# Kernel tuning notes

Hardware: AMD Instinct MI355X
Metric: run time of the kernel (lower is better)

The kernel has to match this reference:

```python
import jax, jax.numpy as jnp
import numpy as np

N_CONCEPTS = 32
D_MODEL = 512
COMMITMENT_COST = 0.25


def setup_inputs() -> dict:
    key = jax.random.key(0)
    kx, kc = jax.random.split(key)
    x = jax.random.normal(kx, (8, 8192, D_MODEL), dtype=jnp.float32)
    codebook = jax.random.normal(kc, (N_CONCEPTS, D_MODEL), dtype=jnp.float32) * 0.02
    return {"x": x, "codebook": codebook}


def reference(x, codebook):
    B, T, D = x.shape
    x_flat = x.reshape(B * T, D)
    x2 = jnp.sum(x_flat * x_flat, axis=1, keepdims=True)          # [BT,1]
    c2 = jnp.sum(codebook * codebook, axis=1)                      # [K]
    xc = jnp.einsum('nd,kd->nk', x_flat, codebook)                 # [BT,K]
    dists = x2 + c2 - 2.0 * xc
    nearest_idx = jnp.argmin(dists, axis=1)                        # [BT]
    q = codebook[nearest_idx]                                      # gather [BT,D]
    # straight-through estimator
    quantized = x_flat + jax.lax.stop_gradient(q - x_flat)
    vq_loss = (jnp.mean((jax.lax.stop_gradient(quantized) - x_flat) ** 2)
               + COMMITMENT_COST * jnp.mean((quantized - jax.lax.stop_gradient(x_flat)) ** 2))
    # histogram of concept usage (fused replacement of the per-concept loop)
    counts = jnp.zeros((N_CONCEPTS,), dtype=jnp.int32).at[nearest_idx].add(1)
    return quantized.reshape(B, T, D), vq_loss, counts
```

## Files before the change

### kernel.cpp

```cpp
#include <hip/hip_runtime.h>

#define BT_ROWS 65536
#define DIM     512
#define NK      32
#define TPB     64
#define RPB     32
#define NBLK    (BT_ROWS / RPB)
#define CHUNK   32
#define NCHUNK  (DIM / CHUNK)
#define DQ      3

typedef float f4 __attribute__((ext_vector_type(4)));
typedef float f32x16 __attribute__((ext_vector_type(16)));
typedef short bf16x8 __attribute__((ext_vector_type(8)));
typedef unsigned int u32x4 __attribute__((ext_vector_type(4)));

union Frag { u32x4 q; unsigned int w[4]; bf16x8 v; };


__global__ void vq_prep(const float* __restrict__ cb, float* __restrict__ c2,
                        int* __restrict__ counts, unsigned int* __restrict__ cbh32) {
    int t = threadIdx.x;
    const f4* c4 = (const f4*)cb;
#pragma unroll
    for (int i = 0; i < 16; ++i) {
        f4 v = c4[t * 16 + i];
        unsigned int w0, w1;
        asm("v_cvt_pk_bf16_f32 %0, %1, %2" : "=v"(w0) : "v"(v.x), "v"(v.y));
        asm("v_cvt_pk_bf16_f32 %0, %1, %2" : "=v"(w1) : "v"(v.z), "v"(v.w));
        cbh32[t * 32 + 2 * i]     = w0;
        cbh32[t * 32 + 2 * i + 1] = w1;
    }
    if (t < NK) {
        float s = 0.f;
#pragma unroll 8
        for (int i = 0; i < DIM / 4; ++i) {
            f4 v = c4[t * (DIM / 4) + i];
            s += v.x * v.x + v.y * v.y + v.z * v.z + v.w * v.w;
        }
        c2[t] = s;
    } else if (t < 2 * NK) {
        counts[t - NK] = 0;
    }
}

__global__ __launch_bounds__(TPB, 2) void vq_main(const float* __restrict__ x,
                                                  const float* __restrict__ cb,
                                                  const float* __restrict__ c2,
                                                  const unsigned short* __restrict__ cbh,
                                                  float* __restrict__ out,
                                                  float* __restrict__ blockloss,
                                                  int* __restrict__ counts) {
    const int lane = threadIdx.x & 63;
    const int n    = lane & 31;
    const int hi   = lane >> 5;
    const int R0   = blockIdx.x * RPB;

    const char* xb = (const char*)x + (size_t)(R0 + n) * (DIM * 4) + hi * 32;
    const unsigned short* cbn = cbh + (size_t)n * DIM + hi * 8;

    f4   rs[DQ][4];
    Frag fr[DQ][2];
#define GLOAD(c) do {                                                    \
    rs[(c) % DQ][0] = *(const f4*)(xb + (c) * 128);                      \
    rs[(c) % DQ][1] = *(const f4*)(xb + (c) * 128 + 16);                 \
    rs[(c) % DQ][2] = *(const f4*)(xb + (c) * 128 + 64);                 \
    rs[(c) % DQ][3] = *(const f4*)(xb + (c) * 128 + 80);                 \
    fr[(c) % DQ][0].q = *(const u32x4*)(cbn + (c) * CHUNK);              \
    fr[(c) % DQ][1].q = *(const u32x4*)(cbn + (c) * CHUNK + 16);         \
} while (0)

    f32x16 acc;
#pragma unroll
    for (int r = 0; r < 16; ++r) acc[r] = 0.f;
    float x2acc = 0.f;

    GLOAD(0); GLOAD(1); GLOAD(2);

#pragma unroll
    for (int c = 0; c < NCHUNK; ++c) {
        f4   a0 = rs[c % DQ][0], a1 = rs[c % DQ][1];
        f4   a2 = rs[c % DQ][2], a3 = rs[c % DQ][3];
        Frag f0 = fr[c % DQ][0], f1 = fr[c % DQ][1];
        if (c + DQ < NCHUNK) GLOAD(c + DQ);

        x2acc += a0.x * a0.x + a0.y * a0.y + a0.z * a0.z + a0.w * a0.w
               + a1.x * a1.x + a1.y * a1.y + a1.z * a1.z + a1.w * a1.w
               + a2.x * a2.x + a2.y * a2.y + a2.z * a2.z + a2.w * a2.w
               + a3.x * a3.x + a3.y * a3.y + a3.z * a3.z + a3.w * a3.w;

        Frag fa;
        asm("v_cvt_pk_bf16_f32 %0, %1, %2" : "=v"(fa.w[0]) : "v"(a0.x), "v"(a0.y));
        asm("v_cvt_pk_bf16_f32 %0, %1, %2" : "=v"(fa.w[1]) : "v"(a0.z), "v"(a0.w));
        asm("v_cvt_pk_bf16_f32 %0, %1, %2" : "=v"(fa.w[2]) : "v"(a1.x), "v"(a1.y));
        asm("v_cvt_pk_bf16_f32 %0, %1, %2" : "=v"(fa.w[3]) : "v"(a1.z), "v"(a1.w));
        acc = __builtin_amdgcn_mfma_f32_32x32x16_bf16(fa.v, f0.v, acc, 0, 0, 0);

        Frag fb;
        asm("v_cvt_pk_bf16_f32 %0, %1, %2" : "=v"(fb.w[0]) : "v"(a2.x), "v"(a2.y));
        asm("v_cvt_pk_bf16_f32 %0, %1, %2" : "=v"(fb.w[1]) : "v"(a2.z), "v"(a2.w));
        asm("v_cvt_pk_bf16_f32 %0, %1, %2" : "=v"(fb.w[2]) : "v"(a3.x), "v"(a3.y));
        asm("v_cvt_pk_bf16_f32 %0, %1, %2" : "=v"(fb.w[3]) : "v"(a3.z), "v"(a3.w));
        acc = __builtin_amdgcn_mfma_f32_32x32x16_bf16(fb.v, f1.v, acc, 0, 0, 0);
    }
#undef GLOAD

    float x2tot = x2acc;
#pragma unroll
    for (int mo = 1; mo <= 32; mo <<= 1) x2tot += __shfl_xor(x2tot, mo, 64);

    const float c2v = c2[n];
    float val[16]; int idx[16];
#pragma unroll
    for (int r = 0; r < 16; ++r) {
        val[r] = c2v - 2.f * acc[r];
        idx[r] = n;
#pragma unroll
        for (int off = 1; off <= 16; off <<= 1) {
            float ov = __shfl_xor(val[r], off, 64);
            int   oi = __shfl_xor(idx[r], off, 64);
            if (ov < val[r] || (ov == val[r] && oi < idx[r])) { val[r] = ov; idx[r] = oi; }
        }
    }

    float lsum = 0.f;
#pragma unroll
    for (int r = 0; r < 16; ++r) lsum += val[r];
    float lother = __shfl(lsum, 32, 64);
    if (lane == 0) blockloss[blockIdx.x] = x2tot + lsum + lother;

    const f4* __restrict__ cb4 = (const f4*)cb;
    f4* __restrict__ o4 = (f4*)out;
    int cnt = 0;
#pragma unroll
    for (int rr = 0; rr < 32; ++rr) {
        const int r = (rr & 3) | (((rr >> 3) & 3) << 2);
        const int h = (rr >> 2) & 1;
        int kr = __shfl(idx[r], h << 5, 64);
        cnt += (kr == n) ? 1 : 0;
        size_t base = (size_t)(R0 + rr) * (DIM / 4);
        o4[base + lane]      = cb4[kr * (DIM / 4) + lane];
        o4[base + 64 + lane] = cb4[kr * (DIM / 4) + 64 + lane];
    }
    if (hi == 0 && cnt) atomicAdd(&counts[n], cnt);

__asm__ volatile("" ::: "memory");
}

__global__ void vq_final(const float* __restrict__ blockloss, const int* __restrict__ counts,
                         float* __restrict__ out) {
    int   t = threadIdx.x;
    float v = 0.f;
#pragma unroll
    for (int i = 0; i < NBLK / 256; ++i) v += blockloss[t + i * 256];
#pragma unroll
    for (int m = 32; m; m >>= 1) v += __shfl_xor(v, m, 64);
    __shared__ float red[4];
    if ((t & 63) == 0) red[t >> 6] = v;
    __syncthreads();
    if (t == 0)
        out[(size_t)BT_ROWS * DIM] =
            1.25f * (red[0] + red[1] + red[2] + red[3]) / (float)((size_t)BT_ROWS * DIM);
    if (t < NK)
        out[(size_t)BT_ROWS * DIM + 1 + t] = (float)counts[t];
}

extern "C" void kernel_launch(void* const* d_in, const int* in_sizes, int n_in,
                              void* d_out, int out_size, void* d_ws, size_t ws_size,
                              hipStream_t stream) {
    const float* x  = (const float*)d_in[0];
    const float* cb = (const float*)d_in[1];
    float* out = (float*)d_out;

    float* f         = (float*)d_ws;
    float* c2        = f;
    float* blockloss = f + NK;
    int*   counts    = (int*)(f + NK + NBLK);
    unsigned int*   cbh32 = (unsigned int*)((char*)d_ws + 16384);
    unsigned short* cbh   = (unsigned short*)cbh32;

    vq_prep<<<1, 256, 0, stream>>>(cb, c2, counts, cbh32);
    vq_main<<<NBLK, TPB, 0, stream>>>(x, cb, c2, cbh, out, blockloss, counts);
    vq_final<<<1, 256, 0, stream>>>(blockloss, counts, out);
}
```

Before: 72.31 us.

## Split reduction dimension across four waves per block and combine via LDS

Each block now runs four wavefronts, each computing MFMA partial dot products over a quarter of the feature dimension. Three waves write their partial accumulators and squared-norm sums to shared memory, and wave 0 combines them before doing the argmin and loss. The gather/write of quantized rows is then split across all four waves using indices passed through shared memory. This raises parallelism and memory-level concurrency per row tile, at the cost of LDS traffic, two block barriers, and a serial section in which only one wave works.

After: 141.2 us. 95.2% more time.

```diff
diff --git a/kernel.cpp b/kernel.cpp
--- a/kernel.cpp
+++ b/kernel.cpp
@@ -3,11 +3,11 @@
 #define BT_ROWS 65536
 #define DIM     512
 #define NK      32
-#define TPB     64
+#define TPB     256
 #define RPB     32
 #define NBLK    (BT_ROWS / RPB)
 #define CHUNK   32
-#define NCHUNK  (DIM / CHUNK)
+#define NCW     4
 #define DQ      3
 
 typedef float f4 __attribute__((ext_vector_type(4)));
@@ -44,20 +44,25 @@
     }
 }
 
-__global__ __launch_bounds__(TPB, 2) void vq_main(const float* __restrict__ x,
+__global__ __launch_bounds__(TPB, 8) void vq_main(const float* __restrict__ x,
                                                   const float* __restrict__ cb,
                                                   const float* __restrict__ c2,
                                                   const unsigned short* __restrict__ cbh,
                                                   float* __restrict__ out,
                                                   float* __restrict__ blockloss,
                                                   int* __restrict__ counts) {
-    const int lane = threadIdx.x & 63;
+    const int tid  = threadIdx.x;
+    const int lane = tid & 63;
+    const int wv   = tid >> 6;
     const int n    = lane & 31;
     const int hi   = lane >> 5;
     const int R0   = blockIdx.x * RPB;
 
-    const char* xb = (const char*)x + (size_t)(R0 + n) * (DIM * 4) + hi * 32;
-    const unsigned short* cbn = cbh + (size_t)n * DIM + hi * 8;
+    __shared__ float         comb[3][17][64];
+    __shared__ unsigned char karr[RPB];
+
+    const char* xb = (const char*)x + (size_t)(R0 + n) * (DIM * 4) + wv * (NCW * CHUNK * 4) + hi * 32;
+    const unsigned short* cbn = cbh + (size_t)n * DIM + wv * (CHUNK * NCW) + hi * 8;
 
     f4   rs[DQ][4];
     Frag fr[DQ][2];
@@ -78,11 +83,11 @@
     GLOAD(0); GLOAD(1); GLOAD(2);
 
 #pragma unroll
-    for (int c = 0; c < NCHUNK; ++c) {
+    for (int c = 0; c < NCW; ++c) {
         f4   a0 = rs[c % DQ][0], a1 = rs[c % DQ][1];
         f4   a2 = rs[c % DQ][2], a3 = rs[c % DQ][3];
         Frag f0 = fr[c % DQ][0], f1 = fr[c % DQ][1];
-        if (c + DQ < NCHUNK) GLOAD(c + DQ);
+        if (c + DQ < NCW) GLOAD(c + DQ);
 
         x2acc += a0.x * a0.x + a0.y * a0.y + a0.z * a0.z + a0.w * a0.w
                + a1.x * a1.x + a1.y * a1.y + a1.z * a1.z + a1.w * a1.w
@@ -105,46 +110,68 @@
     }
 #undef GLOAD
 
-    float x2tot = x2acc;
-#pragma unroll
-    for (int mo = 1; mo <= 32; mo <<= 1) x2tot += __shfl_xor(x2tot, mo, 64);
-
-    const float c2v = c2[n];
-    float val[16]; int idx[16];
-#pragma unroll
-    for (int r = 0; r < 16; ++r) {
-        val[r] = c2v - 2.f * acc[r];
-        idx[r] = n;
-#pragma unroll
-        for (int off = 1; off <= 16; off <<= 1) {
-            float ov = __shfl_xor(val[r], off, 64);
-            int   oi = __shfl_xor(idx[r], off, 64);
-            if (ov < val[r] || (ov == val[r] && oi < idx[r])) { val[r] = ov; idx[r] = oi; }
-        }
-    }
-
-    float lsum = 0.f;
-#pragma unroll
-    for (int r = 0; r < 16; ++r) lsum += val[r];
-    float lother = __shfl(lsum, 32, 64);
-    if (lane == 0) blockloss[blockIdx.x] = x2tot + lsum + lother;
+    if (wv > 0) {
+#pragma unroll
+        for (int r = 0; r < 16; ++r) comb[wv - 1][r][lane] = acc[r];
+        comb[wv - 1][16][lane] = x2acc;
+    }
+    __syncthreads();
+
+    if (wv == 0) {
+#pragma unroll
+        for (int w2 = 0; w2 < 3; ++w2) {
+#pragma unroll
+            for (int r = 0; r < 16; ++r) acc[r] += comb[w2][r][lane];
+            x2acc += comb[w2][16][lane];
+        }
+
+        float x2tot = x2acc;
+#pragma unroll
+        for (int mo = 1; mo <= 32; mo <<= 1) x2tot += __shfl_xor(x2tot, mo, 64);
+
+        const float c2v = c2[n];
+        float val[16]; int idx[16];
+#pragma unroll
+        for (int r = 0; r < 16; ++r) {
+            val[r] = c2v - 2.f * acc[r];
+            idx[r] = n;
+#pragma unroll
+            for (int off = 1; off <= 16; off <<= 1) {
+                float ov = __shfl_xor(val[r], off, 64);
+                int   oi = __shfl_xor(idx[r], off, 64);
+                if (ov < val[r] || (ov == val[r] && oi < idx[r])) { val[r] = ov; idx[r] = oi; }
+            }
+        }
+
+        float lsum = 0.f;
+#pragma unroll
+        for (int r = 0; r < 16; ++r) lsum += val[r];
+        float lother = __shfl(lsum, 32, 64);
+        if (lane == 0) blockloss[blockIdx.x] = x2tot + lsum + lother;
+
+        int cnt = 0;
+#pragma unroll
+        for (int rr = 0; rr < 32; ++rr) {
+            const int r = (rr & 3) | (((rr >> 3) & 3) << 2);
+            const int h = (rr >> 2) & 1;
+            int kr = __shfl(idx[r], h << 5, 64);
+            cnt += (kr == n) ? 1 : 0;
+            if (lane == 0) karr[rr] = (unsigned char)kr;
+        }
+        if (hi == 0 && cnt) atomicAdd(&counts[n], cnt);
+    }
+    __syncthreads();
 
     const f4* __restrict__ cb4 = (const f4*)cb;
     f4* __restrict__ o4 = (f4*)out;
-    int cnt = 0;
-#pragma unroll
-    for (int rr = 0; rr < 32; ++rr) {
-        const int r = (rr & 3) | (((rr >> 3) & 3) << 2);
-        const int h = (rr >> 2) & 1;
-        int kr = __shfl(idx[r], h << 5, 64);
-        cnt += (kr == n) ? 1 : 0;
+#pragma unroll 1
+    for (int rr2 = 0; rr2 < 8; ++rr2) {
+        const int rr = wv * 8 + rr2;
+        int    kr   = karr[rr];
         size_t base = (size_t)(R0 + rr) * (DIM / 4);
         o4[base + lane]      = cb4[kr * (DIM / 4) + lane];
         o4[base + 64 + lane] = cb4[kr * (DIM / 4) + 64 + lane];
     }
-    if (hi == 0 && cnt) atomicAdd(&counts[n], cnt);
-
-__asm__ volatile("" ::: "memory");
 }
 
 __global__ void vq_final(const float* __restrict__ blockloss, const int* __restrict__ counts,
```
